# Optimization experiments

Measured on AMD Instinct MI355X. Metric: run time of the kernel, lower is better.

## Reference

```python
import jax, jax.numpy as jnp
import numpy as np
from jax import lax

LABEL_SIZE = 64
START_ID = 62
PAD_ID = 63
BATCH = 512
SEQ = 512
NEG = -10000.0


def setup_inputs() -> dict:
    key = jax.random.key(0)
    k1, k2, k3, k4 = jax.random.split(key, 4)
    tag_scores = jax.random.normal(k1, (BATCH, SEQ, LABEL_SIZE), dtype=jnp.float32)
    T = 0.1 * jax.random.normal(k2, (LABEL_SIZE, LABEL_SIZE), dtype=jnp.float32)
    # constraints imposed in Model.__init__ on the initial transition matrix
    T = T.at[:, START_ID].set(NEG)
    T = T.at[PAD_ID, :].set(NEG)
    batch_labels = jax.random.randint(k3, (BATCH, SEQ), 0, 62, dtype=jnp.int64)
    lengths = jnp.maximum(jax.random.randint(k4, (BATCH,), 1, SEQ + 1, dtype=jnp.int64), 1)
    return {"tag_scores": tag_scores, "T": T, "batch_labels": batch_labels, "lengths": lengths}


def _crf_loss(tag_scores, T, batch_labels, lengths):
    B, S, L = tag_scores.shape
    mask = jnp.arange(S)[None, :] < lengths[:, None]  # [B,S] contiguous prefix

    # ---- forward algorithm (partition function) ----
    alpha0 = tag_scores[:, 0, :] + T[START_ID, :][None, :]  # [B,L]

    def step(alpha, inp):
        e, m = inp  # e: [B,L] emissions, m: [B] mask
        # scores[b,i,j] = alpha[b,i] + T[i,j] + e[b,j]; reduce over previous label i
        new = jax.nn.logsumexp(alpha[:, :, None] + T[None, :, :] + e[:, None, :], axis=1)
        alpha = jnp.where(m[:, None], new, alpha)
        return alpha, None

    alpha, _ = lax.scan(
        step, alpha0,
        (jnp.swapaxes(tag_scores[:, 1:, :], 0, 1), jnp.swapaxes(mask[:, 1:], 0, 1)),
    )
    final = jax.nn.logsumexp(alpha + T[:, PAD_ID][None, :], axis=1)  # [B]
    forward_scores = final.sum()

    # ---- gold path score ----
    prev = jnp.concatenate(
        [jnp.full((B, 1), START_ID, dtype=batch_labels.dtype), batch_labels[:, :-1]], axis=1
    )  # [B,S]
    trans = T[prev, batch_labels]  # [B,S]
    emit = jnp.take_along_axis(tag_scores, batch_labels[:, :, None], axis=2)[:, :, 0]  # [B,S]
    step_scores = jnp.where(mask, trans + emit, 0.0)
    last_label = jnp.take_along_axis(batch_labels, (lengths - 1)[:, None], axis=1)[:, 0]  # [B]
    gold_scores = step_scores.sum() + T[last_label, PAD_ID].sum()

    return (forward_scores - gold_scores) / B


def reference(tag_scores, T, batch_labels, lengths):
    return _crf_loss(tag_scores, T, batch_labels, lengths)
```

## Files before the change

### kernel.cpp

```cpp
#include <hip/hip_runtime.h>

#define LBL 64
#define SEQN 512
#define BATCHN 512
#define START_ID 62
#define PAD_ID 63
#define CH 8

__global__ __launch_bounds__(64) void crf_batch_kernel(
    const float* __restrict__ ts,
    const float* __restrict__ T,
    const int*   __restrict__ labels,
    const int*   __restrict__ lengths,
    float*       __restrict__ ws)
{
  const int b = blockIdx.x;
  const int j = threadIdx.x;
  const int len = lengths[b];
  const float* __restrict__ e_b = ts + (size_t)b * SEQN * LBL;
  const int* __restrict__ lab_b = labels + b * SEQN;

  const int half = j & 32;
  float c1[32], c2[32];
#pragma unroll
  for (int k = 0; k < 32; ++k) {
    c1[k] = __expf(T[(k + half) * LBL + j]);
    c2[k] = __expf(T[(k + (half ^ 32)) * LBL + j]);
  }
  const float expPad = __expf(T[j * LBL + PAD_ID]);
  const int swap_addr = (j ^ 32) << 2;

  float eC[CH], eNraw[CH];
#pragma unroll
  for (int r = 0; r < CH; ++r) eC[r] = __expf(e_b[r * LBL + j]);
#pragma unroll
  for (int r = 0; r < CH; ++r) eNraw[r] = e_b[(CH + r) * LBL + j];

  float A = __expf(e_b[j] + T[START_ID * LBL + j]);
  int E = 0;

  for (int t0 = 0; t0 < len; t0 += CH) {
#pragma unroll
    for (int tt = 0; tt < CH; ++tt) {
      const int t = t0 + tt;
      if (t >= 1 && t < len) {
        const int Ab = __float_as_int(A);
        const int A2b = __builtin_amdgcn_ds_bpermute(swap_addr, Ab);

        float bc[64];
#define SWZ_PAIR(K)                                                            \
        bc[K]      = __int_as_float(__builtin_amdgcn_ds_swizzle(Ab,  (K) << 5)); \
        bc[32+(K)] = __int_as_float(__builtin_amdgcn_ds_swizzle(A2b, (K) << 5));
        SWZ_PAIR(0)  SWZ_PAIR(1)  SWZ_PAIR(2)  SWZ_PAIR(3)
        SWZ_PAIR(4)  SWZ_PAIR(5)  SWZ_PAIR(6)  SWZ_PAIR(7)
        SWZ_PAIR(8)  SWZ_PAIR(9)  SWZ_PAIR(10) SWZ_PAIR(11)
        SWZ_PAIR(12) SWZ_PAIR(13) SWZ_PAIR(14) SWZ_PAIR(15)
        SWZ_PAIR(16) SWZ_PAIR(17) SWZ_PAIR(18) SWZ_PAIR(19)
        SWZ_PAIR(20) SWZ_PAIR(21) SWZ_PAIR(22) SWZ_PAIR(23)
        SWZ_PAIR(24) SWZ_PAIR(25) SWZ_PAIR(26) SWZ_PAIR(27)
        SWZ_PAIR(28) SWZ_PAIR(29) SWZ_PAIR(30) SWZ_PAIR(31)
#undef SWZ_PAIR

        float s[4] = {0.f, 0.f, 0.f, 0.f};
#pragma unroll
        for (int k = 0; k < 32; ++k)
          s[k & 3] = fmaf(bc[k], c1[k], s[k & 3]);
#pragma unroll
        for (int k = 0; k < 32; ++k)
          s[k & 3] = fmaf(bc[32 + k], c2[k], s[k & 3]);

        float ex = eC[tt];
        if (tt == 0) {
          float m[32];
#pragma unroll
          for (int k = 0; k < 32; ++k) m[k] = fmaxf(bc[k], bc[32 + k]);
#pragma unroll
          for (int st = 16; st >= 1; st >>= 1)
#pragma unroll
            for (int k = 0; k < 16; ++k)
              if (k < st) m[k] = fmaxf(m[k], m[k + st]);
          const unsigned em = (__float_as_uint(m[0]) >> 23) & 255u;
          ex *= __uint_as_float((254u - em) << 23);
          E += 127 - (int)em;
        }
        A = ((s[0] + s[1]) + (s[2] + s[3])) * ex;
      }
    }

#pragma unroll
    for (int r = 0; r < CH; ++r) eC[r] = __expf(eNraw[r]);
    const int tb = (t0 + 2 * CH <= SEQN - CH) ? (t0 + 2 * CH) : (SEQN - CH);
#pragma unroll
    for (int r = 0; r < CH; ++r) eNraw[r] = e_b[(tb + r) * LBL + j];
  }

  float g = 0.0f;
  for (int t = j; t < len; t += 64) {
    const int l = lab_b[t];
    const int prev = (t == 0) ? START_ID : lab_b[t - 1];
    g += T[prev * LBL + l] + e_b[t * LBL + l];
  }

  float v = A * expPad;
#pragma unroll
  for (int d = 1; d < 64; d <<= 1) {
    v += __shfl_xor(v, d);
    g += __shfl_xor(g, d);
  }

  if (j == 0) {
    const int last = lab_b[len - 1];
    const float gold = g + T[last * LBL + PAD_ID];
    const float fwd = logf(v) - (float)E * 0.69314718055994531f;
    ws[b] = fwd - gold;
  }
}

__global__ __launch_bounds__(256) void crf_reduce_kernel(
    const float* __restrict__ ws, float* __restrict__ out)
{
  __shared__ float red[4];
  const int tid = threadIdx.x;
  float v = ws[tid] + ws[tid + 256];
#pragma unroll
  for (int d = 1; d < 64; d <<= 1) v += __shfl_xor(v, d);
  if ((tid & 63) == 0) red[tid >> 6] = v;
  __syncthreads();
  if (tid == 0) out[0] = (red[0] + red[1] + red[2] + red[3]) * (1.0f / BATCHN);
}

extern "C" void kernel_launch(void* const* d_in, const int* in_sizes, int n_in,
                              void* d_out, int out_size, void* d_ws, size_t ws_size,
                              hipStream_t stream) {
  const float* ts      = (const float*)d_in[0];
  const float* T       = (const float*)d_in[1];
  const int*   labels  = (const int*)d_in[2];
  const int*   lengths = (const int*)d_in[3];
  float* out = (float*)d_out;
  float* ws  = (float*)d_ws;

  crf_batch_kernel<<<BATCHN, 64, 0, stream>>>(ts, T, labels, lengths, ws);
  crf_reduce_kernel<<<1, 256, 0, stream>>>(ws, out);
}
```

Baseline: 244.6 us.

## Process two batch rows per wavefront using readlane broadcast for the second chain

Each 64-thread block now runs two independent forward recursions (rows b and b+256) and launches half as many blocks. One chain broadcasts alpha through SGPR readlanes and the other through LDS swizzles, so the scalar and LDS-permute paths can overlap and hide each other's latency. The chunk size drops to 4, with renormalisation still done every 8 steps. In exchange, register pressure rises sharply (a 64-entry c0 array plus two chains), which risks spills, and the loop runs to the longer of the two lengths, which adds wasted steps for the shorter row.

```diff
diff --git a/kernel.cpp b/kernel.cpp
--- a/kernel.cpp
+++ b/kernel.cpp
@@ -5,7 +5,7 @@
 #define BATCHN 512
 #define START_ID 62
 #define PAD_ID 63
-#define CH 8
+#define CH 4
 
 __global__ __launch_bounds__(64) void crf_batch_kernel(
     const float* __restrict__ ts,
@@ -14,11 +14,19 @@
     const int*   __restrict__ lengths,
     float*       __restrict__ ws)
 {
-  const int b = blockIdx.x;
+  const int b0 = blockIdx.x;
+  const int b1 = b0 + (BATCHN / 2);
   const int j = threadIdx.x;
-  const int len = lengths[b];
-  const float* __restrict__ e_b = ts + (size_t)b * SEQN * LBL;
-  const int* __restrict__ lab_b = labels + b * SEQN;
+  const int len0 = lengths[b0];
+  const int len1 = lengths[b1];
+  const float* __restrict__ e0 = ts + (size_t)b0 * SEQN * LBL;
+  const float* __restrict__ e1 = ts + (size_t)b1 * SEQN * LBL;
+  const int* __restrict__ lab0 = labels + b0 * SEQN;
+  const int* __restrict__ lab1 = labels + b1 * SEQN;
+
+  float c0[LBL];
+#pragma unroll
+  for (int i = 0; i < LBL; ++i) c0[i] = __expf(T[i * LBL + j]);
 
   const int half = j & 32;
   float c1[32], c2[32];
@@ -30,27 +38,39 @@
   const float expPad = __expf(T[j * LBL + PAD_ID]);
   const int swap_addr = (j ^ 32) << 2;
 
-  float eC[CH], eNraw[CH];
-#pragma unroll
-  for (int r = 0; r < CH; ++r) eC[r] = __expf(e_b[r * LBL + j]);
-#pragma unroll
-  for (int r = 0; r < CH; ++r) eNraw[r] = e_b[(CH + r) * LBL + j];
-
-  float A = __expf(e_b[j] + T[START_ID * LBL + j]);
-  int E = 0;
-
-  for (int t0 = 0; t0 < len; t0 += CH) {
+  float eC0[CH], eN0[CH], eC1[CH], eN1[CH];
+#pragma unroll
+  for (int r = 0; r < CH; ++r) {
+    eC0[r] = __expf(e0[r * LBL + j]);
+    eC1[r] = __expf(e1[r * LBL + j]);
+  }
+#pragma unroll
+  for (int r = 0; r < CH; ++r) {
+    eN0[r] = e0[(CH + r) * LBL + j];
+    eN1[r] = e1[(CH + r) * LBL + j];
+  }
+
+  float A0 = __expf(e0[j] + T[START_ID * LBL + j]);
+  float A1 = __expf(e1[j] + T[START_ID * LBL + j]);
+  int E0 = 0, E1 = 0;
+
+  const int lenmax = (len0 > len1) ? len0 : len1;
+
+  for (int t0 = 0; t0 < lenmax; t0 += CH) {
+    const bool renorm_chunk = ((t0 & 7) == 0);
 #pragma unroll
     for (int tt = 0; tt < CH; ++tt) {
       const int t = t0 + tt;
-      if (t >= 1 && t < len) {
-        const int Ab = __float_as_int(A);
-        const int A2b = __builtin_amdgcn_ds_bpermute(swap_addr, Ab);
-
+      const bool act0 = (t >= 1) && (t < len0);
+      const bool act1 = (t >= 1) && (t < len1);
+      const bool renorm = renorm_chunk && (tt == 0);
+      if (act0 || act1) {
+        const int A1b = __float_as_int(A1);
+        const int A1s = __builtin_amdgcn_ds_bpermute(swap_addr, A1b);
         float bc[64];
-#define SWZ_PAIR(K)                                                            \
-        bc[K]      = __int_as_float(__builtin_amdgcn_ds_swizzle(Ab,  (K) << 5)); \
-        bc[32+(K)] = __int_as_float(__builtin_amdgcn_ds_swizzle(A2b, (K) << 5));
+#define SWZ_PAIR(K)                                                              \
+        bc[K]      = __int_as_float(__builtin_amdgcn_ds_swizzle(A1b, (K) << 5)); \
+        bc[32+(K)] = __int_as_float(__builtin_amdgcn_ds_swizzle(A1s, (K) << 5));
         SWZ_PAIR(0)  SWZ_PAIR(1)  SWZ_PAIR(2)  SWZ_PAIR(3)
         SWZ_PAIR(4)  SWZ_PAIR(5)  SWZ_PAIR(6)  SWZ_PAIR(7)
         SWZ_PAIR(8)  SWZ_PAIR(9)  SWZ_PAIR(10) SWZ_PAIR(11)
@@ -61,58 +81,113 @@
         SWZ_PAIR(28) SWZ_PAIR(29) SWZ_PAIR(30) SWZ_PAIR(31)
 #undef SWZ_PAIR
 
-        float s[4] = {0.f, 0.f, 0.f, 0.f};
-#pragma unroll
-        for (int k = 0; k < 32; ++k)
-          s[k & 3] = fmaf(bc[k], c1[k], s[k & 3]);
-#pragma unroll
-        for (int k = 0; k < 32; ++k)
-          s[k & 3] = fmaf(bc[32 + k], c2[k], s[k & 3]);
-
-        float ex = eC[tt];
-        if (tt == 0) {
-          float m[32];
-#pragma unroll
-          for (int k = 0; k < 32; ++k) m[k] = fmaxf(bc[k], bc[32 + k]);
+        const int A0b = __float_as_int(A0);
+        int sg[LBL];
+#pragma unroll
+        for (int k = 0; k < LBL; ++k) sg[k] = __builtin_amdgcn_readlane(A0b, k);
+
+        __builtin_amdgcn_sched_barrier(0);
+
+        float s00 = 0.f, s01 = 0.f, s02 = 0.f, s03 = 0.f;
+#pragma unroll
+        for (int k = 0; k < LBL; k += 4) {
+          s00 = fmaf(__int_as_float(sg[k + 0]), c0[k + 0], s00);
+          s01 = fmaf(__int_as_float(sg[k + 1]), c0[k + 1], s01);
+          s02 = fmaf(__int_as_float(sg[k + 2]), c0[k + 2], s02);
+          s03 = fmaf(__int_as_float(sg[k + 3]), c0[k + 3], s03);
+        }
+
+        float s10 = 0.f, s11 = 0.f, s12 = 0.f, s13 = 0.f;
+#pragma unroll
+        for (int k = 0; k < 32; k += 4) {
+          s10 = fmaf(bc[k + 0], c1[k + 0], s10);
+          s11 = fmaf(bc[k + 1], c1[k + 1], s11);
+          s12 = fmaf(bc[k + 2], c1[k + 2], s12);
+          s13 = fmaf(bc[k + 3], c1[k + 3], s13);
+        }
+#pragma unroll
+        for (int k = 0; k < 32; k += 4) {
+          s10 = fmaf(bc[32 + k + 0], c2[k + 0], s10);
+          s11 = fmaf(bc[32 + k + 1], c2[k + 1], s11);
+          s12 = fmaf(bc[32 + k + 2], c2[k + 2], s12);
+          s13 = fmaf(bc[32 + k + 3], c2[k + 3], s13);
+        }
+
+        float ex0 = eC0[tt], ex1 = eC1[tt];
+        if (renorm) {
+          unsigned m[32];
+#pragma unroll
+          for (int k = 0; k < 32; ++k) {
+            const unsigned a = (unsigned)sg[k], bu = (unsigned)sg[k + 32];
+            m[k] = a > bu ? a : bu;
+          }
 #pragma unroll
           for (int st = 16; st >= 1; st >>= 1)
 #pragma unroll
             for (int k = 0; k < 16; ++k)
-              if (k < st) m[k] = fmaxf(m[k], m[k + st]);
-          const unsigned em = (__float_as_uint(m[0]) >> 23) & 255u;
-          ex *= __uint_as_float((254u - em) << 23);
-          E += 127 - (int)em;
-        }
-        A = ((s[0] + s[1]) + (s[2] + s[3])) * ex;
+              if (k < st) m[k] = m[k] > m[k + st] ? m[k] : m[k + st];
+          const unsigned em0 = (m[0] >> 23) & 255u;
+          ex0 *= __uint_as_float((254u - em0) << 23);
+          E0 += act0 ? (127 - (int)em0) : 0;
+
+          float fm[32];
+#pragma unroll
+          for (int k = 0; k < 32; ++k) fm[k] = fmaxf(bc[k], bc[32 + k]);
+#pragma unroll
+          for (int st = 16; st >= 1; st >>= 1)
+#pragma unroll
+            for (int k = 0; k < 16; ++k)
+              if (k < st) fm[k] = fmaxf(fm[k], fm[k + st]);
+          const unsigned em1 = (__float_as_uint(fm[0]) >> 23) & 255u;
+          ex1 *= __uint_as_float((254u - em1) << 23);
+          E1 += act1 ? (127 - (int)em1) : 0;
+        }
+        const float nA0 = ((s00 + s01) + (s02 + s03)) * ex0;
+        const float nA1 = ((s10 + s11) + (s12 + s13)) * ex1;
+        A0 = act0 ? nA0 : A0;
+        A1 = act1 ? nA1 : A1;
       }
     }
 
 #pragma unroll
-    for (int r = 0; r < CH; ++r) eC[r] = __expf(eNraw[r]);
+    for (int r = 0; r < CH; ++r) {
+      eC0[r] = __expf(eN0[r]);
+      eC1[r] = __expf(eN1[r]);
+    }
     const int tb = (t0 + 2 * CH <= SEQN - CH) ? (t0 + 2 * CH) : (SEQN - CH);
 #pragma unroll
-    for (int r = 0; r < CH; ++r) eNraw[r] = e_b[(tb + r) * LBL + j];
-  }
-
-  float g = 0.0f;
-  for (int t = j; t < len; t += 64) {
-    const int l = lab_b[t];
-    const int prev = (t == 0) ? START_ID : lab_b[t - 1];
-    g += T[prev * LBL + l] + e_b[t * LBL + l];
-  }
-
-  float v = A * expPad;
+    for (int r = 0; r < CH; ++r) {
+      eN0[r] = e0[(tb + r) * LBL + j];
+      eN1[r] = e1[(tb + r) * LBL + j];
+    }
+  }
+
+  float g0 = 0.0f, g1 = 0.0f;
+  for (int t = j; t < len0; t += 64) {
+    const int l = lab0[t];
+    const int prev = (t == 0) ? START_ID : lab0[t - 1];
+    g0 += T[prev * LBL + l] + e0[t * LBL + l];
+  }
+  for (int t = j; t < len1; t += 64) {
+    const int l = lab1[t];
+    const int prev = (t == 0) ? START_ID : lab1[t - 1];
+    g1 += T[prev * LBL + l] + e1[t * LBL + l];
+  }
+
+  float v0 = A0 * expPad;
+  float v1 = A1 * expPad;
 #pragma unroll
   for (int d = 1; d < 64; d <<= 1) {
-    v += __shfl_xor(v, d);
-    g += __shfl_xor(g, d);
+    v0 += __shfl_xor(v0, d);
+    g0 += __shfl_xor(g0, d);
+    v1 += __shfl_xor(v1, d);
+    g1 += __shfl_xor(g1, d);
   }
 
   if (j == 0) {
-    const int last = lab_b[len - 1];
-    const float gold = g + T[last * LBL + PAD_ID];
-    const float fwd = logf(v) - (float)E * 0.69314718055994531f;
-    ws[b] = fwd - gold;
+    const float ln2 = 0.69314718055994531f;
+    ws[b0] = (logf(v0) - (float)E0 * ln2) - (g0 + T[lab0[len0 - 1] * LBL + PAD_ID]);
+    ws[b1] = (logf(v1) - (float)E1 * ln2) - (g1 + T[lab1[len1 - 1] * LBL + PAD_ID]);
   }
 }
 
@@ -139,6 +214,6 @@
   float* out = (float*)d_out;
   float* ws  = (float*)d_ws;
 
-  crf_batch_kernel<<<BATCHN, 64, 0, stream>>>(ts, T, labels, lengths, ws);
+  crf_batch_kernel<<<BATCHN / 2, 64, 0, stream>>>(ts, T, labels, lengths, ws);
   crf_reduce_kernel<<<1, 256, 0, stream>>>(ws, out);
 }
```

Result: slower. 415.6 us (+69.9%).
